# Kernel optimization log

Hardware: AMD Instinct MI355X
Metric: run time of the kernel (lower is better)

## Reference

```python
import jax, jax.numpy as jnp
import numpy as np
from jax import lax

# Geometry constants (match init_kwargs): cone-beam, flat panel detector.
W = H = D = 256          # image_size (w, h, d), voxels
NCOL, NROW = 384, 64     # num_det (col, row)
PIX = 1.0                # pix_size (mm)
DET_U, DET_V = 1.2, 1.2  # det_size (col, row) (mm)
ISO, SDD = 500.0, 1000.0 # iso_source, source_detector (mm)
NVIEW = 16
NSAMP = 256              # ray samples across the volume diagonal
RAY_LEN = float(np.sqrt(3.0)) * W * PIX
DT = RAY_LEN / NSAMP     # sampling step along each ray (mm)


def _trilinear(vol, x, y, z):
    """Trilinear sampling of vol [D,H,W] at voxel-index coords (x,y,z); zero outside."""
    x0 = jnp.floor(x); y0 = jnp.floor(y); z0 = jnp.floor(z)
    fx, fy, fz = x - x0, y - y0, z - z0
    x0 = x0.astype(jnp.int32); y0 = y0.astype(jnp.int32); z0 = z0.astype(jnp.int32)

    def fetch(zi, yi, xi):
        inb = (xi >= 0) & (xi < W) & (yi >= 0) & (yi < H) & (zi >= 0) & (zi < D)
        v = vol[jnp.clip(zi, 0, D - 1), jnp.clip(yi, 0, H - 1), jnp.clip(xi, 0, W - 1)]
        return jnp.where(inb, v, jnp.zeros((), vol.dtype))

    out = jnp.zeros(x.shape, vol.dtype)
    for dz, wz in ((0, 1.0 - fz), (1, fz)):
        for dy, wy in ((0, 1.0 - fy), (1, fy)):
            for dx, wx in ((0, 1.0 - fx), (1, fx)):
                out = out + wz * wy * wx * fetch(z0 + dz, y0 + dy, x0 + dx)
    return out


def _project(vol, angles):
    """Cone-beam flat-detector line integrals. vol [D,H,W] -> sino [V,NROW,NCOL]."""
    dt = vol.dtype
    u = ((jnp.arange(NCOL, dtype=dt) - NCOL / 2 + 0.5) * DET_U)  # detector col coords
    v = ((jnp.arange(NROW, dtype=dt) - NROW / 2 + 0.5) * DET_V)  # detector row coords
    t = ISO - RAY_LEN / 2 + (jnp.arange(NSAMP, dtype=dt) + 0.5) * DT  # sample dists

    def one_view(beta):
        cb, sb = jnp.cos(beta), jnp.sin(beta)
        zero = jnp.zeros_like(beta)
        src = jnp.stack([ISO * cb, ISO * sb, zero])          # source position
        ctr = jnp.stack([-(SDD - ISO) * cb, -(SDD - ISO) * sb, zero])  # detector center
        uax = jnp.stack([-sb, cb, zero])                      # detector col axis
        vax = jnp.array([0.0, 0.0, 1.0], dtype=dt)            # detector row axis (z)
        det = ctr + v[:, None, None] * vax + u[None, :, None] * uax   # [NROW,NCOL,3]
        d = det - src
        d = d / jnp.linalg.norm(d, axis=-1, keepdims=True)
        pts = src + t[:, None, None, None] * d[None]          # [S,NROW,NCOL,3]
        vx = pts[..., 0] / PIX + (W - 1) / 2
        vy = pts[..., 1] / PIX + (H - 1) / 2
        vz = pts[..., 2] / PIX + (D - 1) / 2
        return _trilinear(vol, vx, vy, vz).sum(0) * DT        # [NROW,NCOL]

    return lax.map(one_view, angles)                          # [V,NROW,NCOL]


def setup_inputs() -> dict:
    key = jax.random.key(0)
    image = jax.random.normal(key, (1, 1, D, H, W), dtype=jnp.float32)
    angles = jnp.linspace(0.0, 2.0 * np.pi, NVIEW, endpoint=False, dtype=jnp.float32)
    return {"image": image, "angles": angles}


def reference(image, angles):
    # image: [B,C,D,H,W] -> sino: [B,C,V,NROW,NCOL]
    return jax.vmap(jax.vmap(lambda vol: _project(vol, angles)))(image)
```

## Files before the change

### kernel.cpp

```cpp
#include <hip/hip_runtime.h>
#include <hip/hip_fp16.h>
#include <math.h>

namespace {
constexpr int NCOL = 384, NROW = 64, NVIEW = 16, NSAMP = 256;
constexpr float DET_U = 1.2f, DET_V = 1.2f;
constexpr float ISO = 500.0f, SDD = 1000.0f;
constexpr double SQRT3 = 1.7320508075688772;
constexpr float DT = (float)SQRT3;
constexpr float T0 = (float)(500.0 - SQRT3 * 256.0 * 0.5);
constexpr size_t VOL_N = 256u * 256u * 256u;
}

__device__ __forceinline__ void axis_interval(float p0, float d, float LO, float HI,
                                              float& tlo, float& thi) {
    if (fabsf(d) < 1e-7f) {
        if (p0 < LO || p0 > HI) { tlo = 1e30f; thi = -1e30f; }
        else                    { tlo = -1e30f; thi = 1e30f; }
    } else {
        const float r = 1.0f / d;
        const float t1 = (LO - p0) * r, t2 = (HI - p0) * r;
        tlo = fminf(t1, t2); thi = fmaxf(t1, t2);
    }
}

__device__ __forceinline__ float sample_shell(const float* __restrict__ vol,
                                              float vx, float vy, float vz) {
    if (!(vx > -1.0f && vx < 256.0f && vy > -1.0f && vy < 256.0f &&
          vz > -1.0f && vz < 256.0f))
        return 0.0f;
    const float fx0 = floorf(vx), fy0 = floorf(vy), fz0 = floorf(vz);
    const int x0 = (int)fx0, y0 = (int)fy0, z0 = (int)fz0;
    const float fx = vx - fx0, fy = vy - fy0, fz = vz - fz0;
    float sum = 0.0f;
    #pragma unroll
    for (int dzz = 0; dzz < 2; ++dzz) {
        const float wz = dzz ? fz : 1.0f - fz;
        const int zi = z0 + dzz;
        #pragma unroll
        for (int dyy = 0; dyy < 2; ++dyy) {
            const float wy = dyy ? fy : 1.0f - fy;
            const int yi = y0 + dyy;
            #pragma unroll
            for (int dxx = 0; dxx < 2; ++dxx) {
                const float wx = dxx ? fx : 1.0f - fx;
                const int xi = x0 + dxx;
                if ((unsigned)xi < 256u && (unsigned)yi < 256u && (unsigned)zi < 256u)
                    sum += wz * wy * wx * vol[(zi << 16) | (yi << 8) | xi];
            }
        }
    }
    return sum;
}

struct Spans { int g0, s0, s1, g1; float dx, dy, dz, bx, by, bz; float cb, sb; };

__device__ __forceinline__ Spans ray_setup(const float* __restrict__ angles, int tid) {
    Spans sp;
    const int col = tid % NCOL;
    const int rv  = tid / NCOL;
    const int row = rv % NROW;
    const int view = rv / NROW;

    const float beta = angles[view];
    const float cb = cosf(beta), sb = sinf(beta);
    sp.cb = cb; sp.sb = sb;
    const float u = (col - NCOL * 0.5f + 0.5f) * DET_U;
    const float v = (row - NROW * 0.5f + 0.5f) * DET_V;

    const float sx = ISO * cb, sy = ISO * sb;
    const float detx = -(SDD - ISO) * cb - u * sb;
    const float dety = -(SDD - ISO) * sb + u * cb;
    const float detz = v;

    float dx = detx - sx, dy = dety - sy, dz = detz;
    const float inv = 1.0f / sqrtf(dx * dx + dy * dy + dz * dz);
    dx *= inv; dy *= inv; dz *= inv;
    sp.dx = dx; sp.dy = dy; sp.dz = dz;
    sp.bx = sx + 127.5f; sp.by = sy + 127.5f; sp.bz = 127.5f;

    float xl, xh, yl, yh, zl, zh;
    axis_interval(sp.bx, dx, 0.01f, 254.99f, xl, xh);
    axis_interval(sp.by, dy, 0.01f, 254.99f, yl, yh);
    axis_interval(sp.bz, dz, 0.01f, 254.99f, zl, zh);
    const float tin  = fmaxf(xl, fmaxf(yl, zl));
    const float tout = fminf(xh, fminf(yh, zh));

    axis_interval(sp.bx, dx, -1.05f, 256.05f, xl, xh);
    axis_interval(sp.by, dy, -1.05f, 256.05f, yl, yh);
    axis_interval(sp.bz, dz, -1.05f, 256.05f, zl, zh);
    const float glo = fmaxf(xl, fmaxf(yl, zl));
    const float ghi = fminf(xh, fminf(yh, zh));

    const float invdt = 1.0f / DT;
    float g0f = floorf((glo - T0) * invdt - 0.5f);
    float g1f = ceilf((ghi - T0) * invdt - 0.5f) + 1.0f;
    float s0f = ceilf((tin - T0) * invdt - 0.5f + 0.01f);
    float s1f = floorf((tout - T0) * invdt - 0.5f - 0.01f) + 1.0f;
    int g0 = (int)fminf(fmaxf(g0f, 0.0f), 256.0f);
    int g1 = (int)fminf(fmaxf(g1f, 0.0f), 256.0f);
    int s0 = (int)fminf(fmaxf(s0f, 0.0f), 256.0f);
    int s1 = (int)fminf(fmaxf(s1f, 0.0f), 256.0f);
    s0 = max(s0, g0); s1 = min(s1, g1);
    if (s1 < s0) { s0 = g0; s1 = g0; }
    sp.g0 = g0; sp.s0 = s0; sp.s1 = s1; sp.g1 = g1;
    return sp;
}

__global__ __launch_bounds__(256) void packP_kernel(const float* __restrict__ vol,
                                                    __half2* __restrict__ P) {
    const unsigned i = blockIdx.x * 256u + threadIdx.x;
    const unsigned z = i >> 16;
    const float a = vol[i];
    const float b = (z < 255u) ? vol[i + 65536] : a;
    P[i] = __floats2half2_rn(a, b);
}

__global__ __launch_bounds__(256) void packPT_kernel(const float* __restrict__ vol,
                                                     __half2* __restrict__ PT) {
    __shared__ __half2 tile[32][33];
    const int z = blockIdx.z;
    const int z1 = (z < 255) ? z + 1 : 255;
    const int x0 = blockIdx.x * 32, y0 = blockIdx.y * 32;
    const int tx = threadIdx.x, ty = threadIdx.y;
    const float* s0 = vol + (z  << 16);
    const float* s1 = vol + (z1 << 16);
    #pragma unroll
    for (int i = 0; i < 32; i += 8) {
        const int idx = ((y0 + ty + i) << 8) | (x0 + tx);
        tile[ty + i][tx] = __floats2half2_rn(s0[idx], s1[idx]);
    }
    __syncthreads();
    __half2* d = PT + (z << 16);
    #pragma unroll
    for (int i = 0; i < 32; i += 8)
        d[((x0 + ty + i) << 8) | (y0 + tx)] = tile[tx][ty + i];
}

__device__ __forceinline__ float zlerp(__half2 q, float fc) {
    const float lo = __low2float(q), hi = __high2float(q);
    return fmaf(fc, hi - lo, lo);
}

__global__ __launch_bounds__(256) void projector3d_zp_kernel(
    const float* __restrict__ vol,
    const __half2* __restrict__ P,
    const __half2* __restrict__ PT,
    const float* __restrict__ angles,
    float* __restrict__ out)
{
    const int tid = blockIdx.x * 256 + threadIdx.x;

    const Spans sp = ray_setup(angles, tid);
    const float dx = sp.dx, dy = sp.dy, dz = sp.dz;
    const float bx = sp.bx, by = sp.by, bz = sp.bz;

    const bool useT = fabsf(sp.cb) > fabsf(sp.sb);
    const __half2* __restrict__ Pm = useT ? PT : P;
    const float da = useT ? dy : dx, db = useT ? dx : dy;
    const float ba = useT ? by : bx, bb = useT ? bx : by;

    float acc = 0.0f;

    for (int s = sp.g0; s < sp.s0; ++s) {
        const float t = T0 + (s + 0.5f) * DT;
        acc += sample_shell(vol, fmaf(t, dx, bx), fmaf(t, dy, by), fmaf(t, dz, bz));
    }

    int s = sp.s0;
    if (s < sp.s1) {
        float t = T0 + (s + 0.5f) * DT;
        float va = fmaf(t, da, ba), vb = fmaf(t, db, bb), vc = fmaf(t, dz, bz);
        float fa0 = floorf(va), fb0 = floorf(vb), fc0 = floorf(vc);
        float fa = va - fa0, fb = vb - fb0, fc = vc - fc0;
        const __half2* p = Pm + (((int)fc0 << 16) | ((int)fb0 << 8) | (int)fa0);
        __half2 q00 = p[0], q01 = p[1], q10 = p[256], q11 = p[257];

        for (++s; s < sp.s1; ++s) {
            t = T0 + (s + 0.5f) * DT;
            const float nva = fmaf(t, da, ba), nvb = fmaf(t, db, bb), nvc = fmaf(t, dz, bz);
            const float nfa0 = floorf(nva), nfb0 = floorf(nvb), nfc0 = floorf(nvc);
            const __half2* np = Pm + (((int)nfc0 << 16) | ((int)nfb0 << 8) | (int)nfa0);
            const __half2 nq00 = np[0], nq01 = np[1], nq10 = np[256], nq11 = np[257];

            const float v00 = zlerp(q00, fc), v01 = zlerp(q01, fc);
            const float v10 = zlerp(q10, fc), v11 = zlerp(q11, fc);
            const float ca0 = fmaf(fa, v01 - v00, v00);
            const float ca1 = fmaf(fa, v11 - v10, v10);
            acc += fmaf(fb, ca1 - ca0, ca0);

            fa = nva - nfa0; fb = nvb - nfb0; fc = nvc - nfc0;
            q00 = nq00; q01 = nq01; q10 = nq10; q11 = nq11;
        }
        const float v00 = zlerp(q00, fc), v01 = zlerp(q01, fc);
        const float v10 = zlerp(q10, fc), v11 = zlerp(q11, fc);
        const float ca0 = fmaf(fa, v01 - v00, v00);
        const float ca1 = fmaf(fa, v11 - v10, v10);
        acc += fmaf(fb, ca1 - ca0, ca0);
    }

    for (int s2 = sp.s1; s2 < sp.g1; ++s2) {
        const float t = T0 + (s2 + 0.5f) * DT;
        acc += sample_shell(vol, fmaf(t, dx, bx), fmaf(t, dy, by), fmaf(t, dz, bz));
    }

    out[tid] = acc * DT;
}

__global__ __launch_bounds__(256) void transpose_kernel(const float* __restrict__ vol,
                                                        float* __restrict__ volT) {
    __shared__ float tile[32][33];
    const int z = blockIdx.z;
    const int x0 = blockIdx.x * 32, y0 = blockIdx.y * 32;
    const int tx = threadIdx.x, ty = threadIdx.y;
    const float* src = vol + (z << 16);
    float* dst = volT + (z << 16);
    #pragma unroll
    for (int i = 0; i < 32; i += 8)
        tile[ty + i][tx] = src[((y0 + ty + i) << 8) | (x0 + tx)];
    __syncthreads();
    #pragma unroll
    for (int i = 0; i < 32; i += 8)
        dst[((x0 + ty + i) << 8) | (y0 + tx)] = tile[tx][ty + i];
}

__global__ __launch_bounds__(256) void projector3d_dual_kernel(
    const float* __restrict__ vol, const float* __restrict__ volT,
    const float* __restrict__ angles, float* __restrict__ out)
{
    const int tid = blockIdx.x * 256 + threadIdx.x;
    const Spans sp = ray_setup(angles, tid);
    const float dx = sp.dx, dy = sp.dy, dz = sp.dz;
    const float bx = sp.bx, by = sp.by, bz = sp.bz;
    const bool useT = fabsf(sp.cb) > fabsf(sp.sb);
    const float* __restrict__ Pm = useT ? volT : vol;
    const float da = useT ? dy : dx, db = useT ? dx : dy;
    const float ba = useT ? by : bx, bb = useT ? bx : by;

    float acc = 0.0f;
    for (int s = sp.g0; s < sp.s0; ++s) {
        const float t = T0 + (s + 0.5f) * DT;
        acc += sample_shell(vol, fmaf(t, dx, bx), fmaf(t, dy, by), fmaf(t, dz, bz));
    }
    for (int s = sp.s0; s < sp.s1; ++s) {
        const float t = T0 + (s + 0.5f) * DT;
        const float va = fmaf(t, da, ba), vb = fmaf(t, db, bb), vc = fmaf(t, dz, bz);
        const float fa0 = floorf(va), fb0 = floorf(vb), fc0 = floorf(vc);
        const float fa = va - fa0, fb = vb - fb0, fc = vc - fc0;
        const float* p = Pm + (((int)fc0 << 16) | ((int)fb0 << 8) | (int)fa0);
        const float v000 = p[0],     v001 = p[1];
        const float v010 = p[256],   v011 = p[257];
        const float v100 = p[65536], v101 = p[65537];
        const float v110 = p[65792], v111 = p[65793];
        const float c00 = fmaf(fa, v001 - v000, v000);
        const float c01 = fmaf(fa, v011 - v010, v010);
        const float c10 = fmaf(fa, v101 - v100, v100);
        const float c11 = fmaf(fa, v111 - v110, v110);
        const float c0 = fmaf(fb, c01 - c00, c00);
        const float c1 = fmaf(fb, c11 - c10, c10);
        acc += fmaf(fc, c1 - c0, c0);
    }
    for (int s = sp.s1; s < sp.g1; ++s) {
        const float t = T0 + (s + 0.5f) * DT;
        acc += sample_shell(vol, fmaf(t, dx, bx), fmaf(t, dy, by), fmaf(t, dz, bz));
    }
    out[tid] = acc * DT;
}

__global__ __launch_bounds__(256) void projector3d_f32_kernel(
    const float* __restrict__ vol, const float* __restrict__ angles,
    float* __restrict__ out)
{
    const int tid = blockIdx.x * 256 + threadIdx.x;
    const Spans sp = ray_setup(angles, tid);
    const float dx = sp.dx, dy = sp.dy, dz = sp.dz;
    const float bx = sp.bx, by = sp.by, bz = sp.bz;
    float acc = 0.0f;
    for (int s = sp.g0; s < sp.s0; ++s) {
        const float t = T0 + (s + 0.5f) * DT;
        acc += sample_shell(vol, fmaf(t, dx, bx), fmaf(t, dy, by), fmaf(t, dz, bz));
    }
    #pragma unroll 4
    for (int s = sp.s0; s < sp.s1; ++s) {
        const float t = T0 + (s + 0.5f) * DT;
        const float vx = fmaf(t, dx, bx), vy = fmaf(t, dy, by), vz = fmaf(t, dz, bz);
        const float fx0 = floorf(vx), fy0 = floorf(vy), fz0 = floorf(vz);
        const int x0 = (int)fx0, y0 = (int)fy0, z0 = (int)fz0;
        const float fx = vx - fx0, fy = vy - fy0, fz = vz - fz0;
        const float* p = vol + ((z0 << 16) | (y0 << 8) | x0);
        const float v000 = p[0],     v001 = p[1];
        const float v010 = p[256],   v011 = p[257];
        const float v100 = p[65536], v101 = p[65537];
        const float v110 = p[65792], v111 = p[65793];
        const float c00 = fmaf(fx, v001 - v000, v000);
        const float c01 = fmaf(fx, v011 - v010, v010);
        const float c10 = fmaf(fx, v101 - v100, v100);
        const float c11 = fmaf(fx, v111 - v110, v110);
        const float c0 = fmaf(fy, c01 - c00, c00);
        const float c1 = fmaf(fy, c11 - c10, c10);
        acc += fmaf(fz, c1 - c0, c0);
    }
    for (int s = sp.s1; s < sp.g1; ++s) {
        const float t = T0 + (s + 0.5f) * DT;
        acc += sample_shell(vol, fmaf(t, dx, bx), fmaf(t, dy, by), fmaf(t, dz, bz));
    }
    out[tid] = acc * DT;
}

extern "C" void kernel_launch(void* const* d_in, const int* in_sizes, int n_in,
                              void* d_out, int out_size, void* d_ws, size_t ws_size,
                              hipStream_t stream) {
    const float* vol    = (const float*)d_in[0];
    const float* angles = (const float*)d_in[1];
    float* out = (float*)d_out;

    const int grid = (NVIEW * NROW * NCOL) / 256;
    if (ws_size >= 2u * VOL_N * sizeof(__half2) / 1) {
        __half2* P  = (__half2*)d_ws;
        __half2* PT = P + VOL_N;
        packP_kernel<<<(int)(VOL_N / 256), 256, 0, stream>>>(vol, P);
        dim3 tgrid(8, 8, 256), tblk(32, 8);
        packPT_kernel<<<tgrid, tblk, 0, stream>>>(vol, PT);
        projector3d_zp_kernel<<<grid, 256, 0, stream>>>(vol, P, PT, angles, out);
    } else if (ws_size >= VOL_N * sizeof(float)) {
        float* volT = (float*)d_ws;
        dim3 tgrid(8, 8, 256), tblk(32, 8);
        transpose_kernel<<<tgrid, tblk, 0, stream>>>(vol, volT);
        projector3d_dual_kernel<<<grid, 256, 0, stream>>>(vol, volT, angles, out);
    } else {
        projector3d_f32_kernel<<<grid, 256, 0, stream>>>(vol, angles, out);
    }
}
```

Measured before the change: 264.7 us.

## Fuse packing kernels and double-buffer interior ray sample loads

Merges the two half2 packing kernels into one that writes both the plain and the transposed z-pair layouts from a single read of the volume, which cuts one kernel launch and one full pass over the source. The interior ray loop now keeps two samples' gathers in flight (ping-pong A/B) instead of one, to hide more of the gather latency. The cost is more live registers per thread, which may reduce occupancy.

```diff
diff --git a/kernel.cpp b/kernel.cpp
--- a/kernel.cpp
+++ b/kernel.cpp
@@ -107,17 +107,9 @@
     return sp;
 }
 
-__global__ __launch_bounds__(256) void packP_kernel(const float* __restrict__ vol,
-                                                    __half2* __restrict__ P) {
-    const unsigned i = blockIdx.x * 256u + threadIdx.x;
-    const unsigned z = i >> 16;
-    const float a = vol[i];
-    const float b = (z < 255u) ? vol[i + 65536] : a;
-    P[i] = __floats2half2_rn(a, b);
-}
-
-__global__ __launch_bounds__(256) void packPT_kernel(const float* __restrict__ vol,
-                                                     __half2* __restrict__ PT) {
+__global__ __launch_bounds__(256) void packBoth_kernel(const float* __restrict__ vol,
+                                                       __half2* __restrict__ P,
+                                                       __half2* __restrict__ PT) {
     __shared__ __half2 tile[32][33];
     const int z = blockIdx.z;
     const int z1 = (z < 255) ? z + 1 : 255;
@@ -125,22 +117,27 @@
     const int tx = threadIdx.x, ty = threadIdx.y;
     const float* s0 = vol + (z  << 16);
     const float* s1 = vol + (z1 << 16);
+    __half2* Pp = P + (z << 16);
     #pragma unroll
     for (int i = 0; i < 32; i += 8) {
         const int idx = ((y0 + ty + i) << 8) | (x0 + tx);
-        tile[ty + i][tx] = __floats2half2_rn(s0[idx], s1[idx]);
+        const __half2 h = __floats2half2_rn(s0[idx], s1[idx]);
+        Pp[idx] = h;
+        tile[ty + i][tx] = h;
     }
     __syncthreads();
-    __half2* d = PT + (z << 16);
+    __half2* Tp = PT + (z << 16);
     #pragma unroll
     for (int i = 0; i < 32; i += 8)
-        d[((x0 + ty + i) << 8) | (y0 + tx)] = tile[tx][ty + i];
+        Tp[((x0 + ty + i) << 8) | (y0 + tx)] = tile[tx][ty + i];
 }
 
 __device__ __forceinline__ float zlerp(__half2 q, float fc) {
     const float lo = __low2float(q), hi = __high2float(q);
     return fmaf(fc, hi - lo, lo);
 }
+
+struct Smp { float fa, fb, fc; __half2 q00, q01, q10, q11; };
 
 __global__ __launch_bounds__(256) void projector3d_zp_kernel(
     const float* __restrict__ vol,
@@ -167,36 +164,47 @@
         acc += sample_shell(vol, fmaf(t, dx, bx), fmaf(t, dy, by), fmaf(t, dz, bz));
     }
 
-    int s = sp.s0;
-    if (s < sp.s1) {
-        float t = T0 + (s + 0.5f) * DT;
-        float va = fmaf(t, da, ba), vb = fmaf(t, db, bb), vc = fmaf(t, dz, bz);
-        float fa0 = floorf(va), fb0 = floorf(vb), fc0 = floorf(vc);
-        float fa = va - fa0, fb = vb - fb0, fc = vc - fc0;
-        const __half2* p = Pm + (((int)fc0 << 16) | ((int)fb0 << 8) | (int)fa0);
-        __half2 q00 = p[0], q01 = p[1], q10 = p[256], q11 = p[257];
-
-        for (++s; s < sp.s1; ++s) {
-            t = T0 + (s + 0.5f) * DT;
-            const float nva = fmaf(t, da, ba), nvb = fmaf(t, db, bb), nvc = fmaf(t, dz, bz);
-            const float nfa0 = floorf(nva), nfb0 = floorf(nvb), nfc0 = floorf(nvc);
-            const __half2* np = Pm + (((int)nfc0 << 16) | ((int)nfb0 << 8) | (int)nfa0);
-            const __half2 nq00 = np[0], nq01 = np[1], nq10 = np[256], nq11 = np[257];
-
-            const float v00 = zlerp(q00, fc), v01 = zlerp(q01, fc);
-            const float v10 = zlerp(q10, fc), v11 = zlerp(q11, fc);
-            const float ca0 = fmaf(fa, v01 - v00, v00);
-            const float ca1 = fmaf(fa, v11 - v10, v10);
-            acc += fmaf(fb, ca1 - ca0, ca0);
-
-            fa = nva - nfa0; fb = nvb - nfb0; fc = nvc - nfc0;
-            q00 = nq00; q01 = nq01; q10 = nq10; q11 = nq11;
+    auto LOADS = [&](Smp& S, int si) {
+        const float t = T0 + (si + 0.5f) * DT;
+        const float va = fmaf(t, da, ba), vb = fmaf(t, db, bb), vc = fmaf(t, dz, bz);
+        const float a0 = floorf(va), b0 = floorf(vb), c0 = floorf(vc);
+        S.fa = va - a0; S.fb = vb - b0; S.fc = vc - c0;
+        const __half2* p = Pm + (((int)c0 << 16) | ((int)b0 << 8) | (int)a0);
+        S.q00 = p[0]; S.q01 = p[1]; S.q10 = p[256]; S.q11 = p[257];
+    };
+    auto CONS = [&](const Smp& S) -> float {
+        const float v00 = zlerp(S.q00, S.fc), v01 = zlerp(S.q01, S.fc);
+        const float v10 = zlerp(S.q10, S.fc), v11 = zlerp(S.q11, S.fc);
+        const float c0 = fmaf(S.fa, v01 - v00, v00);
+        const float c1 = fmaf(S.fa, v11 - v10, v10);
+        return fmaf(S.fb, c1 - c0, c0);
+    };
+
+    {
+        int s = sp.s0;
+        const int s1 = sp.s1;
+        if (s < s1) {
+            Smp A, B;
+            LOADS(A, s);
+            if (s + 1 < s1) {
+                LOADS(B, s + 1);
+                s += 2;
+                for (; s + 1 < s1; s += 2) {
+                    acc += CONS(A); LOADS(A, s);
+                    acc += CONS(B); LOADS(B, s + 1);
+                }
+                if (s < s1) {
+                    acc += CONS(A); LOADS(A, s);
+                    acc += CONS(B);
+                    acc += CONS(A);
+                } else {
+                    acc += CONS(A);
+                    acc += CONS(B);
+                }
+            } else {
+                acc += CONS(A);
+            }
         }
-        const float v00 = zlerp(q00, fc), v01 = zlerp(q01, fc);
-        const float v10 = zlerp(q10, fc), v11 = zlerp(q11, fc);
-        const float ca0 = fmaf(fa, v01 - v00, v00);
-        const float ca1 = fmaf(fa, v11 - v10, v10);
-        acc += fmaf(fb, ca1 - ca0, ca0);
     }
 
     for (int s2 = sp.s1; s2 < sp.g1; ++s2) {
@@ -315,12 +323,11 @@
     float* out = (float*)d_out;
 
     const int grid = (NVIEW * NROW * NCOL) / 256;
-    if (ws_size >= 2u * VOL_N * sizeof(__half2) / 1) {
+    if (ws_size >= 2u * VOL_N * sizeof(__half2)) {
         __half2* P  = (__half2*)d_ws;
         __half2* PT = P + VOL_N;
-        packP_kernel<<<(int)(VOL_N / 256), 256, 0, stream>>>(vol, P);
         dim3 tgrid(8, 8, 256), tblk(32, 8);
-        packPT_kernel<<<tgrid, tblk, 0, stream>>>(vol, PT);
+        packBoth_kernel<<<tgrid, tblk, 0, stream>>>(vol, P, PT);
         projector3d_zp_kernel<<<grid, 256, 0, stream>>>(vol, P, PT, angles, out);
     } else if (ws_size >= VOL_N * sizeof(float)) {
         float* volT = (float*)d_ws;
```

Measured after the change: 255.0 us. 3.7% less time.
